# Kernel tuning notes

Measured on AMD Instinct MI355X. Metric: run time of the kernel, lower is better.

Reference implementation:

```python
import jax, jax.numpy as jnp
import numpy as np


def _lstm(x, W_ih, W_hh, b_ih, b_hh):
    """PyTorch-convention LSTM. x: [B, T, I] -> (ys [B, T, H], h_T [B, H]).
    Gate order i, f, g, o as in torch.nn.LSTM."""
    def step(carry, xt):
        h, c = carry
        gates = xt @ W_ih.T + b_ih + h @ W_hh.T + b_hh
        i, f, g, o = jnp.split(gates, 4, axis=-1)
        c = jax.nn.sigmoid(f) * c + jax.nn.sigmoid(i) * jnp.tanh(g)
        h = jax.nn.sigmoid(o) * jnp.tanh(c)
        return (h, c), h
    B = x.shape[0]
    H = W_hh.shape[1]
    init = (jnp.zeros((B, H), x.dtype), jnp.zeros((B, H), x.dtype))
    (hT, _), ys = jax.lax.scan(step, init, jnp.swapaxes(x, 0, 1))
    return jnp.swapaxes(ys, 0, 1), hT


def setup_inputs():
    key = jax.random.key(0)
    ks = jax.random.split(key, 13)
    B, S, F = 256, 1024, 16
    p = lambda k, shape: jax.random.normal(k, shape, jnp.float32) * 0.1
    return {
        "x": jax.random.normal(ks[0], (B, S, F), jnp.float32),
        "data": 0,
        "W_ih1": p(ks[1], (32, 1)),  "W_hh1": p(ks[2], (32, 8)),
        "b_ih1": p(ks[3], (32,)),    "b_hh1": p(ks[4], (32,)),
        "W_ih2": p(ks[5], (512, 8)), "W_hh2": p(ks[6], (512, 128)),
        "b_ih2": p(ks[7], (512,)),   "b_hh2": p(ks[8], (512,)),
        "W1": p(ks[9], (64, 128)),   "b1": p(ks[10], (64,)),
        "W2": p(ks[11], (1, 64)),    "b2": p(ks[12], (1,)),
    }


def reference(x, data, W_ih1, W_hh1, b_ih1, b_hh1,
              W_ih2, W_hh2, b_ih2, b_hh2, W1, b1, W2, b2):
    B, S, F = x.shape
    # rnn1: original loops over batch; here all B*S rows are one big batch of
    # length-F sequences with feature dim 1. We only need the final hidden h_T.
    x1 = x.reshape(B * S, F, 1)
    _, h1 = _lstm(x1, W_ih1, W_hh1, b_ih1, b_hh1)            # [B*S, 8]
    # original does .detach().numpy() -> gradient is cut here
    h1 = jax.lax.stop_gradient(h1).reshape(B, S, 8)
    ys2, _ = _lstm(h1, W_ih2, W_hh2, b_ih2, b_hh2)           # [B, S, 128]
    last = ys2[:, -1, :]                                     # [B, 128]
    return (last @ W1.T + b1) @ W2.T + b2                    # [B, 1]
```

## Files before the change

### kernel.cpp

```cpp
#include <hip/hip_runtime.h>
#include <cstdint>

typedef _Float16 f16x2 __attribute__((ext_vector_type(2)));

__device__ __forceinline__ float fsig(float x) {
  return __fdividef(1.f, 1.f + __expf(-x));
}
__device__ __forceinline__ float ftanh_(float x) {
  return fmaf(2.f, fsig(x + x), -1.f);
}
__device__ __forceinline__ int packf16(float a, float b) {
  f16x2 p; p.x = (_Float16)a; p.y = (_Float16)b;
  return __builtin_bit_cast(int, p);
}
__device__ __forceinline__ float dot2(int w, int h, float acc) {
  return __builtin_amdgcn_fdot2(__builtin_bit_cast(f16x2, w),
                                __builtin_bit_cast(f16x2, h), acc, false);
}
template <int CTRL>
__device__ __forceinline__ float qp(float v) {
  return __int_as_float(__builtin_amdgcn_update_dpp(
      0, __float_as_int(v), CTRL, 0xF, 0xF, true));
}
#define QP_X1 0xB1
#define QP_X2 0x4E

__global__ __launch_bounds__(256, 2) void lstm1_kernel(
    const float* __restrict__ x, const float* __restrict__ Wih,
    const float* __restrict__ Whh, const float* __restrict__ bih,
    const float* __restrict__ bhh, int4* __restrict__ h1out) {
  const int n = blockIdx.x * 256 + threadIdx.x;

  int whh2[128];
#pragma unroll
  for (int r = 0; r < 32; ++r) {
#pragma unroll
    for (int j = 0; j < 4; ++j) {
      float2 v = ((const float2*)(Whh + r * 8))[j];
      whh2[r * 4 + j] = packf16(v.x, v.y);
    }
  }
  int wxb[32];
#pragma unroll
  for (int r = 0; r < 32; ++r) wxb[r] = packf16(Wih[r], bih[r] + bhh[r]);

#pragma unroll
  for (int i = 0; i < 128; i += 8)
    asm volatile("" : "+v"(whh2[i]), "+v"(whh2[i + 1]), "+v"(whh2[i + 2]),
                      "+v"(whh2[i + 3]), "+v"(whh2[i + 4]), "+v"(whh2[i + 5]),
                      "+v"(whh2[i + 6]), "+v"(whh2[i + 7]));
#pragma unroll
  for (int i = 0; i < 32; i += 8)
    asm volatile("" : "+v"(wxb[i]), "+v"(wxb[i + 1]), "+v"(wxb[i + 2]),
                      "+v"(wxb[i + 3]), "+v"(wxb[i + 4]), "+v"(wxb[i + 5]),
                      "+v"(wxb[i + 6]), "+v"(wxb[i + 7]));

  const float4* __restrict__ xp4 = (const float4*)(x + (size_t)n * 16);
  float c[8];
  int h2[4];
#pragma unroll
  for (int k = 0; k < 8; ++k) c[k] = 0.f;
#pragma unroll
  for (int j = 0; j < 4; ++j) h2[j] = 0;

  float4 xcur = xp4[0];
#pragma unroll 1
  for (int tt = 0; tt < 4; ++tt) {
    float4 xnxt = xp4[(tt + 1) & 3];
    float xs[4] = {xcur.x, xcur.y, xcur.z, xcur.w};
#pragma unroll
    for (int u = 0; u < 4; ++u) {
      const int xt1 = packf16(xs[u], 1.f);
      float hn[8];
#pragma unroll
      for (int k = 0; k < 8; ++k) {
        float acc[4];
#pragma unroll
        for (int gi = 0; gi < 4; ++gi) {
          const int r = gi * 8 + k;
          float a = dot2(wxb[r], xt1, 0.f);
          a = dot2(whh2[r * 4 + 0], h2[0], a);
          a = dot2(whh2[r * 4 + 1], h2[1], a);
          a = dot2(whh2[r * 4 + 2], h2[2], a);
          a = dot2(whh2[r * 4 + 3], h2[3], a);
          acc[gi] = a;
        }
        float iv = fsig(acc[0]), fv = fsig(acc[1]);
        float gv = ftanh_(acc[2]), ov = fsig(acc[3]);
        c[k] = fmaf(fv, c[k], iv * gv);
        hn[k] = ov * ftanh_(c[k]);
      }
#pragma unroll
      for (int j = 0; j < 4; ++j) h2[j] = packf16(hn[2 * j], hn[2 * j + 1]);
    }
    xcur = xnxt;
  }
  int4 o;
  o.x = h2[0]; o.y = h2[1]; o.z = h2[2]; o.w = h2[3];
  h1out[n] = o;
}

__global__ __launch_bounds__(512, 1) void lstm2_kernel(
    const int4* __restrict__ h1, const float* __restrict__ Wih,
    const float* __restrict__ Whh, const float* __restrict__ bih,
    const float* __restrict__ bhh, const float* __restrict__ Wd1,
    const float* __restrict__ bd1, const float* __restrict__ Wd2,
    const float* __restrict__ bd2, float* __restrict__ out) {
  __shared__ __align__(16) _Float16 sH[2][128];
  const int b = blockIdx.x;
  const int t = threadIdx.x;
  const int m = t >> 2;
  const int q = t & 3;
  const int G = ((q & 1) << 1) | (q >> 1);
  const bool sel0 = (q & 1) != 0;
  const bool sel1 = (q & 2) != 0;
  const bool isq0 = (q == 0);
  const bool isq1 = (q == 1);

  int w[64];
#pragma unroll
  for (int g = 0; g < 4; ++g) {
    const float2* p = (const float2*)(Whh + (size_t)(g * 128 + m) * 128 + q * 32);
#pragma unroll
    for (int j = 0; j < 16; ++j) {
      float2 v = p[j];
      w[g * 16 + j] = packf16(v.x, v.y);
    }
  }

  int wig[4];
  {
    const float2* pi = (const float2*)(Wih + (size_t)(G * 128 + m) * 8);
#pragma unroll
    for (int j = 0; j < 4; ++j) {
      float2 v = pi[j];
      wig[j] = packf16(v.x, v.y);
    }
  }
  const float bias = bih[G * 128 + m] + bhh[G * 128 + m];

  int hq[16];
#pragma unroll
  for (int i = 0; i < 16; ++i) hq[i] = 0;
  float c = 0.f;

  const int4* __restrict__ xg = h1 + (size_t)b * 1024;
  int4 xc = xg[0];
  int4 xn = xg[1];

#pragma unroll 1
  for (int ts = 0; ts < 1024; ++ts) {
#pragma unroll
    for (int i = 0; i < 64; i += 8)
      asm volatile("" : "+v"(w[i]), "+v"(w[i + 1]), "+v"(w[i + 2]),
                        "+v"(w[i + 3]), "+v"(w[i + 4]), "+v"(w[i + 5]),
                        "+v"(w[i + 6]), "+v"(w[i + 7]));
    asm volatile("" : "+v"(wig[0]), "+v"(wig[1]), "+v"(wig[2]), "+v"(wig[3]));

    float bx = bias;
    bx = dot2(wig[0], xc.x, bx);
    bx = dot2(wig[1], xc.y, bx);
    bx = dot2(wig[2], xc.z, bx);
    bx = dot2(wig[3], xc.w, bx);

    float R0 = 0.f, R1 = 0.f, R2 = 0.f, R3 = 0.f;
#pragma unroll
    for (int j = 0; j < 16; ++j) {
      R0 = dot2(w[j], hq[j], R0);
      R1 = dot2(w[16 + j], hq[j], R1);
      R2 = dot2(w[32 + j], hq[j], R2);
      R3 = dot2(w[48 + j], hq[j], R3);
    }
    float s0 = sel0 ? R0 : R2, s1 = sel0 ? R1 : R3;
    float k0 = sel0 ? R2 : R0, k1 = sel0 ? R3 : R1;
    float S0 = k0 + qp<QP_X1>(s0);
    float S1 = k1 + qp<QP_X1>(s1);
    float s2 = sel1 ? S0 : S1;
    float k2 = sel1 ? S1 : S0;
    float S = k2 + qp<QP_X2>(s2) + bx;

    float u = isq1 ? (S + S) : S;
    float sg = fsig(u);
    float act = isq1 ? fmaf(2.f, sg, -1.f) : sg;

    float v0 = act;
    float v1 = qp<QP_X1>(v0);
    float v2 = qp<QP_X2>(v0);
    float v3 = qp<QP_X2>(v1);
    float p01 = sel0 ? v1 : v0, p23 = sel0 ? v3 : v2;
    float q01 = sel0 ? v0 : v1, q23 = sel0 ? v2 : v3;
    float iv = sel1 ? p23 : p01;
    float fv = sel1 ? p01 : p23;
    float gv = sel1 ? q23 : q01;
    float ov = sel1 ? q01 : q23;

    c = fmaf(fv, c, iv * gv);
    float hx = ov * ftanh_(c);
    if (isq0) sH[ts & 1][m] = (_Float16)hx;
    __syncthreads();

    {
      const int4* src = (const int4*)(&sH[ts & 1][q * 32]);
      int4 A = src[0], B = src[1], C = src[2], D = src[3];
      hq[0] = A.x;  hq[1] = A.y;  hq[2] = A.z;  hq[3] = A.w;
      hq[4] = B.x;  hq[5] = B.y;  hq[6] = B.z;  hq[7] = B.w;
      hq[8] = C.x;  hq[9] = C.y;  hq[10] = C.z; hq[11] = C.w;
      hq[12] = D.x; hq[13] = D.y; hq[14] = D.z; hq[15] = D.w;
      xc = xn;
      xn = xg[ts < 1022 ? ts + 2 : 1023];
    }
  }

  if (t < 64) {
    float a = bd1[t];
#pragma unroll
    for (int k = 0; k < 128; ++k)
      a = fmaf(Wd1[t * 128 + k], (float)sH[1][k], a);
    float v = a * Wd2[t];
#pragma unroll
    for (int off = 32; off > 0; off >>= 1) v += __shfl_down(v, off);
    if (t == 0) out[b] = v + bd2[0];
  }
}

extern "C" void kernel_launch(void* const* d_in, const int* in_sizes, int n_in,
                              void* d_out, int out_size, void* d_ws, size_t ws_size,
                              hipStream_t stream) {
  const float* x    = (const float*)d_in[0];
  const float* Wih1 = (const float*)d_in[2];
  const float* Whh1 = (const float*)d_in[3];
  const float* bih1 = (const float*)d_in[4];
  const float* bhh1 = (const float*)d_in[5];
  const float* Wih2 = (const float*)d_in[6];
  const float* Whh2 = (const float*)d_in[7];
  const float* bih2 = (const float*)d_in[8];
  const float* bhh2 = (const float*)d_in[9];
  const float* W1   = (const float*)d_in[10];
  const float* b1   = (const float*)d_in[11];
  const float* W2   = (const float*)d_in[12];
  const float* b2   = (const float*)d_in[13];
  float* out = (float*)d_out;

  int4* h1 = (int4*)d_ws;

  lstm1_kernel<<<1024, 256, 0, stream>>>(x, Wih1, Whh1, bih1, bhh1, h1);
  lstm2_kernel<<<256, 512, 0, stream>>>(h1, Wih2, Whh2, bih2, bhh2,
                                        W1, b1, W2, b2, out);
}
```

Baseline: 817.3 us.

## Split LSTM2 work across thread pairs instead of quads, halving block size

The second LSTM now assigns each hidden unit to two threads, each covering half of the hidden-state reduction for all four gates, instead of four threads. This removes one DPP reduction/broadcast stage and halves the number of waves synchronizing per timestep, at the cost of doubling per-thread dot-product work and register use. The first LSTM loop is also restructured to load scalar inputs per step rather than float4 chunks.

```diff
diff --git a/kernel.cpp b/kernel.cpp
--- a/kernel.cpp
+++ b/kernel.cpp
@@ -23,7 +23,6 @@
       0, __float_as_int(v), CTRL, 0xF, 0xF, true));
 }
 #define QP_X1 0xB1
-#define QP_X2 0x4E
 
 __global__ __launch_bounds__(256, 2) void lstm1_kernel(
     const float* __restrict__ x, const float* __restrict__ Wih,
@@ -55,7 +54,7 @@
                       "+v"(wxb[i + 3]), "+v"(wxb[i + 4]), "+v"(wxb[i + 5]),
                       "+v"(wxb[i + 6]), "+v"(wxb[i + 7]));
 
-  const float4* __restrict__ xp4 = (const float4*)(x + (size_t)n * 16);
+  const float* __restrict__ xp = x + (size_t)n * 16;
   float c[8];
   int h2[4];
 #pragma unroll
@@ -63,44 +62,40 @@
 #pragma unroll
   for (int j = 0; j < 4; ++j) h2[j] = 0;
 
-  float4 xcur = xp4[0];
+  float xv = xp[0];
 #pragma unroll 1
-  for (int tt = 0; tt < 4; ++tt) {
-    float4 xnxt = xp4[(tt + 1) & 3];
-    float xs[4] = {xcur.x, xcur.y, xcur.z, xcur.w};
-#pragma unroll
-    for (int u = 0; u < 4; ++u) {
-      const int xt1 = packf16(xs[u], 1.f);
-      float hn[8];
-#pragma unroll
-      for (int k = 0; k < 8; ++k) {
-        float acc[4];
-#pragma unroll
-        for (int gi = 0; gi < 4; ++gi) {
-          const int r = gi * 8 + k;
-          float a = dot2(wxb[r], xt1, 0.f);
-          a = dot2(whh2[r * 4 + 0], h2[0], a);
-          a = dot2(whh2[r * 4 + 1], h2[1], a);
-          a = dot2(whh2[r * 4 + 2], h2[2], a);
-          a = dot2(whh2[r * 4 + 3], h2[3], a);
-          acc[gi] = a;
-        }
-        float iv = fsig(acc[0]), fv = fsig(acc[1]);
-        float gv = ftanh_(acc[2]), ov = fsig(acc[3]);
-        c[k] = fmaf(fv, c[k], iv * gv);
-        hn[k] = ov * ftanh_(c[k]);
+  for (int t = 0; t < 16; ++t) {
+    float xn = xp[(t + 1) & 15];
+    const int xt1 = packf16(xv, 1.f);
+    float hn[8];
+#pragma unroll
+    for (int k = 0; k < 8; ++k) {
+      float acc[4];
+#pragma unroll
+      for (int gi = 0; gi < 4; ++gi) {
+        const int r = gi * 8 + k;
+        float a = dot2(wxb[r], xt1, 0.f);
+        a = dot2(whh2[r * 4 + 0], h2[0], a);
+        a = dot2(whh2[r * 4 + 1], h2[1], a);
+        a = dot2(whh2[r * 4 + 2], h2[2], a);
+        a = dot2(whh2[r * 4 + 3], h2[3], a);
+        acc[gi] = a;
       }
-#pragma unroll
-      for (int j = 0; j < 4; ++j) h2[j] = packf16(hn[2 * j], hn[2 * j + 1]);
-    }
-    xcur = xnxt;
+      float iv = fsig(acc[0]), fv = fsig(acc[1]);
+      float gv = ftanh_(acc[2]), ov = fsig(acc[3]);
+      c[k] = fmaf(fv, c[k], iv * gv);
+      hn[k] = ov * ftanh_(c[k]);
+    }
+#pragma unroll
+    for (int j = 0; j < 4; ++j) h2[j] = packf16(hn[2 * j], hn[2 * j + 1]);
+    xv = xn;
   }
   int4 o;
   o.x = h2[0]; o.y = h2[1]; o.z = h2[2]; o.w = h2[3];
   h1out[n] = o;
 }
 
-__global__ __launch_bounds__(512, 1) void lstm2_kernel(
+__global__ __launch_bounds__(256, 1) void lstm2_kernel(
     const int4* __restrict__ h1, const float* __restrict__ Wih,
     const float* __restrict__ Whh, const float* __restrict__ bih,
     const float* __restrict__ bhh, const float* __restrict__ Wd1,
@@ -109,39 +104,46 @@
   __shared__ __align__(16) _Float16 sH[2][128];
   const int b = blockIdx.x;
   const int t = threadIdx.x;
-  const int m = t >> 2;
-  const int q = t & 3;
-  const int G = ((q & 1) << 1) | (q >> 1);
-  const bool sel0 = (q & 1) != 0;
-  const bool sel1 = (q & 2) != 0;
-  const bool isq0 = (q == 0);
+  const int m = t >> 1;
+  const int q = t & 1;
   const bool isq1 = (q == 1);
 
-  int w[64];
+  int w[128];
 #pragma unroll
   for (int g = 0; g < 4; ++g) {
-    const float2* p = (const float2*)(Whh + (size_t)(g * 128 + m) * 128 + q * 32);
-#pragma unroll
-    for (int j = 0; j < 16; ++j) {
+    const float2* p = (const float2*)(Whh + (size_t)(g * 128 + m) * 128 + q * 64);
+#pragma unroll
+    for (int j = 0; j < 32; ++j) {
       float2 v = p[j];
-      w[g * 16 + j] = packf16(v.x, v.y);
-    }
-  }
-
-  int wig[4];
+      w[g * 32 + j] = packf16(v.x, v.y);
+    }
+  }
+#pragma unroll
+  for (int i = 0; i < 128; i += 8)
+    asm volatile("" : "+v"(w[i]), "+v"(w[i + 1]), "+v"(w[i + 2]),
+                      "+v"(w[i + 3]), "+v"(w[i + 4]), "+v"(w[i + 5]),
+                      "+v"(w[i + 6]), "+v"(w[i + 7]));
+
+  int wigA[4], wigB[4];
+  float biasA, biasB;
   {
-    const float2* pi = (const float2*)(Wih + (size_t)(G * 128 + m) * 8);
+    const int rowA = (2 * q) * 128 + m;
+    const int rowB = (2 * q + 1) * 128 + m;
+    const float2* pa = (const float2*)(Wih + (size_t)rowA * 8);
+    const float2* pb = (const float2*)(Wih + (size_t)rowB * 8);
 #pragma unroll
     for (int j = 0; j < 4; ++j) {
-      float2 v = pi[j];
-      wig[j] = packf16(v.x, v.y);
-    }
-  }
-  const float bias = bih[G * 128 + m] + bhh[G * 128 + m];
-
-  int hq[16];
-#pragma unroll
-  for (int i = 0; i < 16; ++i) hq[i] = 0;
+      float2 va = pa[j], vb = pb[j];
+      wigA[j] = packf16(va.x, va.y);
+      wigB[j] = packf16(vb.x, vb.y);
+    }
+    biasA = bih[rowA] + bhh[rowA];
+    biasB = bih[rowB] + bhh[rowB];
+  }
+
+  int hq[32];
+#pragma unroll
+  for (int i = 0; i < 32; ++i) hq[i] = 0;
   float c = 0.f;
 
   const int4* __restrict__ xg = h1 + (size_t)b * 1024;
@@ -150,62 +152,69 @@
 
 #pragma unroll 1
   for (int ts = 0; ts < 1024; ++ts) {
-#pragma unroll
-    for (int i = 0; i < 64; i += 8)
-      asm volatile("" : "+v"(w[i]), "+v"(w[i + 1]), "+v"(w[i + 2]),
-                        "+v"(w[i + 3]), "+v"(w[i + 4]), "+v"(w[i + 5]),
-                        "+v"(w[i + 6]), "+v"(w[i + 7]));
-    asm volatile("" : "+v"(wig[0]), "+v"(wig[1]), "+v"(wig[2]), "+v"(wig[3]));
-
-    float bx = bias;
-    bx = dot2(wig[0], xc.x, bx);
-    bx = dot2(wig[1], xc.y, bx);
-    bx = dot2(wig[2], xc.z, bx);
-    bx = dot2(wig[3], xc.w, bx);
-
-    float R0 = 0.f, R1 = 0.f, R2 = 0.f, R3 = 0.f;
+    float bxA = biasA, bxB = biasB;
+    bxA = dot2(wigA[0], xc.x, bxA);
+    bxA = dot2(wigA[1], xc.y, bxA);
+    bxA = dot2(wigA[2], xc.z, bxA);
+    bxA = dot2(wigA[3], xc.w, bxA);
+    bxB = dot2(wigB[0], xc.x, bxB);
+    bxB = dot2(wigB[1], xc.y, bxB);
+    bxB = dot2(wigB[2], xc.z, bxB);
+    bxB = dot2(wigB[3], xc.w, bxB);
+
+    float R0a = 0.f, R1a = 0.f, R2a = 0.f, R3a = 0.f;
+    float R0b = 0.f, R1b = 0.f, R2b = 0.f, R3b = 0.f;
 #pragma unroll
     for (int j = 0; j < 16; ++j) {
-      R0 = dot2(w[j], hq[j], R0);
-      R1 = dot2(w[16 + j], hq[j], R1);
-      R2 = dot2(w[32 + j], hq[j], R2);
-      R3 = dot2(w[48 + j], hq[j], R3);
-    }
-    float s0 = sel0 ? R0 : R2, s1 = sel0 ? R1 : R3;
-    float k0 = sel0 ? R2 : R0, k1 = sel0 ? R3 : R1;
-    float S0 = k0 + qp<QP_X1>(s0);
-    float S1 = k1 + qp<QP_X1>(s1);
-    float s2 = sel1 ? S0 : S1;
-    float k2 = sel1 ? S1 : S0;
-    float S = k2 + qp<QP_X2>(s2) + bx;
-
-    float u = isq1 ? (S + S) : S;
-    float sg = fsig(u);
-    float act = isq1 ? fmaf(2.f, sg, -1.f) : sg;
-
-    float v0 = act;
-    float v1 = qp<QP_X1>(v0);
-    float v2 = qp<QP_X2>(v0);
-    float v3 = qp<QP_X2>(v1);
-    float p01 = sel0 ? v1 : v0, p23 = sel0 ? v3 : v2;
-    float q01 = sel0 ? v0 : v1, q23 = sel0 ? v2 : v3;
-    float iv = sel1 ? p23 : p01;
-    float fv = sel1 ? p01 : p23;
-    float gv = sel1 ? q23 : q01;
-    float ov = sel1 ? q01 : q23;
+      R0a = dot2(w[j], hq[j], R0a);
+      R1a = dot2(w[32 + j], hq[j], R1a);
+      R2a = dot2(w[64 + j], hq[j], R2a);
+      R3a = dot2(w[96 + j], hq[j], R3a);
+    }
+#pragma unroll
+    for (int j = 16; j < 32; ++j) {
+      R0b = dot2(w[j], hq[j], R0b);
+      R1b = dot2(w[32 + j], hq[j], R1b);
+      R2b = dot2(w[64 + j], hq[j], R2b);
+      R3b = dot2(w[96 + j], hq[j], R3b);
+    }
+    float R0 = R0a + R0b, R1 = R1a + R1b;
+    float R2 = R2a + R2b, R3 = R3a + R3b;
+
+    float vA = isq1 ? R0 : R2;
+    float Sa = (isq1 ? R2 : R0) + qp<QP_X1>(vA) + bxA;
+    float vB = isq1 ? R1 : R3;
+    float Sb = (isq1 ? R3 : R1) + qp<QP_X1>(vB) + bxB;
+
+    float ua = isq1 ? (Sa + Sa) : Sa;
+    float sga = fsig(ua);
+    float actA = isq1 ? fmaf(2.f, sga, -1.f) : sga;
+    float actB = fsig(Sb);
+
+    float ga = qp<QP_X1>(actA);
+    float gb = qp<QP_X1>(actB);
+    float iv = isq1 ? ga : actA;
+    float gv = isq1 ? actA : ga;
+    float fv = isq1 ? gb : actB;
+    float ov = isq1 ? actB : gb;
 
     c = fmaf(fv, c, iv * gv);
     float hx = ov * ftanh_(c);
-    if (isq0) sH[ts & 1][m] = (_Float16)hx;
+    if (!isq1) sH[ts & 1][m] = (_Float16)hx;
     __syncthreads();
 
     {
-      const int4* src = (const int4*)(&sH[ts & 1][q * 32]);
+      const int4* src = (const int4*)(&sH[ts & 1][q * 64]);
       int4 A = src[0], B = src[1], C = src[2], D = src[3];
-      hq[0] = A.x;  hq[1] = A.y;  hq[2] = A.z;  hq[3] = A.w;
-      hq[4] = B.x;  hq[5] = B.y;  hq[6] = B.z;  hq[7] = B.w;
-      hq[8] = C.x;  hq[9] = C.y;  hq[10] = C.z; hq[11] = C.w;
-      hq[12] = D.x; hq[13] = D.y; hq[14] = D.z; hq[15] = D.w;
+      int4 E = src[4], F = src[5], G2 = src[6], H = src[7];
+      hq[0] = A.x;   hq[1] = A.y;   hq[2] = A.z;   hq[3] = A.w;
+      hq[4] = B.x;   hq[5] = B.y;   hq[6] = B.z;   hq[7] = B.w;
+      hq[8] = C.x;   hq[9] = C.y;   hq[10] = C.z;  hq[11] = C.w;
+      hq[12] = D.x;  hq[13] = D.y;  hq[14] = D.z;  hq[15] = D.w;
+      hq[16] = E.x;  hq[17] = E.y;  hq[18] = E.z;  hq[19] = E.w;
+      hq[20] = F.x;  hq[21] = F.y;  hq[22] = F.z;  hq[23] = F.w;
+      hq[24] = G2.x; hq[25] = G2.y; hq[26] = G2.z; hq[27] = G2.w;
+      hq[28] = H.x;  hq[29] = H.y;  hq[30] = H.z;  hq[31] = H.w;
       xc = xn;
       xn = xg[ts < 1022 ? ts + 2 : 1023];
     }
@@ -244,6 +253,6 @@
   int4* h1 = (int4*)d_ws;
 
   lstm1_kernel<<<1024, 256, 0, stream>>>(x, Wih1, Whh1, bih1, bhh1, h1);
-  lstm2_kernel<<<256, 512, 0, stream>>>(h1, Wih2, Whh2, bih2, bhh2,
+  lstm2_kernel<<<256, 256, 0, stream>>>(h1, Wih2, Whh2, bih2, bhh2,
                                         W1, b1, W2, b2, out);
 }
```

New measurement: 786.4 us. -3.8%, faster.
